# Kernel optimization log

Hardware: AMD Instinct MI355X
Metric: run time of the kernel (lower is better)

The kernel has to match this reference:

```python
import jax, jax.numpy as jnp
import numpy as np

B, C, H, W = 32, 512, 32, 32


def setup_inputs() -> dict:
    key = jax.random.key(0)
    ks = jax.random.split(key, 7)
    c2 = C // 2
    s_in = (1.0 / C) ** 0.5   # torch Conv2d default init scale (kernel 1x1)
    s_c2 = (1.0 / c2) ** 0.5
    return {
        "x": jax.random.normal(ks[0], (B, C, H, W), jnp.float32),
        "Wk": jax.random.normal(ks[1], (c2, C), jnp.float32) * s_in,
        "bk": jax.random.normal(ks[2], (c2,), jnp.float32) * s_in,
        "Wv": jax.random.normal(ks[3], (c2, C), jnp.float32) * s_in,
        "bv": jax.random.normal(ks[4], (c2,), jnp.float32) * s_in,
        "Wo": jax.random.normal(ks[5], (C, c2), jnp.float32) * s_c2,
        "bo": jax.random.normal(ks[6], (C,), jnp.float32) * s_c2,
    }


def reference(x, Wk, bk, Wv, bv, Wo, bo):
    Bn, Cn, Hn, Wn = x.shape
    c2 = Cn // 2
    M = Hn * Wn
    # 1x1 convs as channel contractions
    k = jnp.einsum('oc,bchw->bohw', Wk, x) + bk[None, :, None, None]   # [B,c2,H,W]
    v = jnp.einsum('oc,bchw->bohw', Wv, x) + bv[None, :, None, None]   # [B,c2,H,W]
    # torch .reshape(B, M, c2) reinterprets memory (NOT a transpose) -> same in jnp
    v = v.reshape(Bn, M, c2)                                           # [B,M,c2]
    kf = k.reshape(Bn, c2, M)                                          # [B,c2,M]
    # cov_feature: k^T I_hat k with I_hat = (1/M)I - (1/M^2)11^T
    #            = (1/M) k^T k - (1/M^2) s s^T,  s = sum over channels
    gram = jnp.einsum('bcm,bcn->bmn', kf, kf) / M                      # [B,M,M]
    s = kf.sum(axis=1)                                                 # [B,M]
    cov = gram - (s[:, :, None] * s[:, None, :]) / (M * M)
    attn = jax.nn.softmax(cov * (c2 ** -0.5), axis=-1)                 # [B,M,M]
    out = jnp.einsum('bmn,bnc->bmc', attn, v)                          # [B,M,c2]
    # torch .view(B, c2, H, W) is also a raw memory reinterpretation
    out = out.reshape(Bn, c2, Hn, Wn)
    out = jnp.einsum('oc,bchw->bohw', Wo, out) + bo[None, :, None, None]
    return out + x
```

## Files before the change

### kernel.cpp

```cpp
#include <hip/hip_runtime.h>


typedef short bf8 __attribute__((ext_vector_type(8)));
typedef float f32x4 __attribute__((ext_vector_type(4)));

#define MFMA16(a, b, c) __builtin_amdgcn_mfma_f32_16x16x32_bf16((a), (b), (c), 0, 0, 0)

__device__ __forceinline__ short f2bf(float x) {
  unsigned u = __float_as_uint(x);
  u += 0x7fffu + ((u >> 16) & 1u);
  return (short)(u >> 16);
}

__device__ __forceinline__ void gll16(const short* g, void* l) {
  __builtin_amdgcn_global_load_lds(
      (const __attribute__((address_space(1))) unsigned int*)g,
      (__attribute__((address_space(3))) unsigned int*)l, 16, 0, 0);
}

__device__ __forceinline__ void gemm_core(const short* __restrict__ A,
                                          const short* __restrict__ B,
                                          int ldA, int ldB, int ksteps,
                                          char* smem, f32x4 acc[4][4]) {
  const int tid = threadIdx.x;
  const int w = tid >> 6, l = tid & 63;
  const int q = l >> 4, i = l & 15;
  const int wm = w & 1, wn = w >> 1;
  const int srow = l >> 3;
  const int gcol = ((l & 7) ^ srow) * 8;
  f32x4 zz = {0.f, 0.f, 0.f, 0.f};
  #pragma unroll
  for (int mt = 0; mt < 4; ++mt)
    #pragma unroll
    for (int nt = 0; nt < 4; ++nt) acc[mt][nt] = zz;

  for (int ks = 0; ks < ksteps; ++ks) {
    __syncthreads();
    const short* Ak = A + ks * 64 + gcol;
    const short* Bk = B + ks * 64 + gcol;
    #pragma unroll
    for (int j = 0; j < 4; ++j) {
      int s = w * 4 + j;
      size_t row = (size_t)(s * 8 + srow);
      gll16(Ak + row * ldA, smem + s * 1024);
      gll16(Bk + row * ldB, smem + 16384 + s * 1024);
    }
    __syncthreads();
    #pragma unroll
    for (int kq = 0; kq < 2; ++kq) {
      int sw = ((kq * 4 + q) ^ (i & 7)) * 16;
      bf8 af[4], bq[4];
      #pragma unroll
      for (int mt = 0; mt < 4; ++mt)
        af[mt] = *(const bf8*)(smem + (wm * 64 + mt * 16 + i) * 128 + sw);
      #pragma unroll
      for (int nt = 0; nt < 4; ++nt)
        bq[nt] = *(const bf8*)(smem + 16384 + (wn * 64 + nt * 16 + i) * 128 + sw);
      #pragma unroll
      for (int mt = 0; mt < 4; ++mt)
        #pragma unroll
        for (int nt = 0; nt < 4; ++nt)
          acc[mt][nt] = MFMA16(af[mt], bq[nt], acc[mt][nt]);
    }
  }
}

__global__ __launch_bounds__(256) void p0_xpose(const float* __restrict__ x,
                                                short* __restrict__ xT) {
  __shared__ float lds[64][65];
  int cb = blockIdx.x, sb = blockIdx.y, b = blockIdx.z;
  int t = threadIdx.x;
  int c0 = cb * 64, sp0 = sb * 64;
  const float4* x4 = reinterpret_cast<const float4*>(x);
  #pragma unroll
  for (int j = 0; j < 4; ++j) {
    int lin = t + 256 * j;
    int cl = lin >> 4, s4 = lin & 15;
    float4 v = x4[(((size_t)b * 512 + c0 + cl) * 1024 + sp0 + s4 * 4) >> 2];
    lds[cl][s4 * 4 + 0] = v.x; lds[cl][s4 * 4 + 1] = v.y;
    lds[cl][s4 * 4 + 2] = v.z; lds[cl][s4 * 4 + 3] = v.w;
  }
  __syncthreads();
  int spl = t >> 2, cs = (t & 3) * 16;
  bf8 o0, o1;
  #pragma unroll
  for (int j = 0; j < 8; ++j) o0[j] = f2bf(lds[cs + j][spl]);
  #pragma unroll
  for (int j = 0; j < 8; ++j) o1[j] = f2bf(lds[cs + 8 + j][spl]);
  size_t base = ((size_t)b * 1024 + sp0 + spl) * 512 + c0 + cs;
  *reinterpret_cast<bf8*>(xT + base) = o0;
  *reinterpret_cast<bf8*>(xT + base + 8) = o1;
}

__global__ __launch_bounds__(256) void w0_weights(const float* __restrict__ Wk,
                                                  const float* __restrict__ Wv,
                                                  const float* __restrict__ Wo,
                                                  short* __restrict__ Wkv_bf,
                                                  short* __restrict__ Wo_bf) {
  int g = blockIdx.x * 256 + threadIdx.x;
  if (g < 262144) {
    int o = g >> 9, c = g & 511;
    float v = (o < 256) ? Wk[o * 512 + c] : Wv[(o - 256) * 512 + c];
    Wkv_bf[g] = f2bf(v);
  } else {
    int i2 = g - 262144;
    Wo_bf[i2] = f2bf(Wo[i2]);
  }
}

__global__ __launch_bounds__(256, 2) void k1_kv(const short* __restrict__ xT,
                                                const short* __restrict__ Wkv,
                                                const float* __restrict__ bk,
                                                const float* __restrict__ bv,
                                                short* __restrict__ kT,
                                                short* __restrict__ vT,
                                                float* __restrict__ s_part) {
  __shared__ __attribute__((aligned(16))) char smem[32768];
  f32x4 acc[4][4];
  int bm = blockIdx.x, bn = blockIdx.y;
  gemm_core(xT + (size_t)bm * 128 * 512, Wkv + (size_t)bn * 128 * 512,
            512, 512, 8, smem, acc);
  int tid = threadIdx.x;
  int w = tid >> 6, l = tid & 63, q = l >> 4, i = l & 15;
  int wm = w & 1, wn = w >> 1;
  int mbase = bm * 128 + wm * 64;
  int nbase = bn * 128 + wn * 64;
  if (bn < 2) {
    float rp[4][4];
    #pragma unroll
    for (int mt = 0; mt < 4; ++mt)
      #pragma unroll
      for (int r = 0; r < 4; ++r) rp[mt][r] = 0.f;
    #pragma unroll
    for (int mt = 0; mt < 4; ++mt)
      #pragma unroll
      for (int nt = 0; nt < 4; ++nt) {
        float bias = bk[nbase + nt * 16 + i];
        #pragma unroll
        for (int r = 0; r < 4; ++r) {
          float val = acc[mt][nt][r] + bias;
          int mg = mbase + mt * 16 + q * 4 + r;
          kT[(size_t)mg * 256 + nbase + nt * 16 + i] = f2bf(val);
          rp[mt][r] += val;
        }
      }
    #pragma unroll
    for (int mask = 1; mask <= 8; mask <<= 1)
      #pragma unroll
      for (int mt = 0; mt < 4; ++mt)
        #pragma unroll
        for (int r = 0; r < 4; ++r) rp[mt][r] += __shfl_xor(rp[mt][r], mask, 64);
    if (i == 0) {
      int pg = bn * 2 + wn;
      #pragma unroll
      for (int mt = 0; mt < 4; ++mt)
        #pragma unroll
        for (int r = 0; r < 4; ++r)
          s_part[pg * 32768 + mbase + mt * 16 + q * 4 + r] = rp[mt][r];
    }
  } else {
    #pragma unroll
    for (int mt = 0; mt < 4; ++mt)
      #pragma unroll
      for (int nt = 0; nt < 4; ++nt) {
        int o2 = nbase + nt * 16 + i - 256;
        float bias = bv[o2];
        #pragma unroll
        for (int r = 0; r < 4; ++r) {
          float val = acc[mt][nt][r] + bias;
          int mg = mbase + mt * 16 + q * 4 + r;
          int b = mg >> 10, sp = mg & 1023;
          vT[((size_t)b * 256 + (sp & 255)) * 1024 + 4 * o2 + (sp >> 8)] = f2bf(val);
        }
      }
  }
}

__global__ __launch_bounds__(256) void k1b_sum(const float* __restrict__ s_part,
                                               float* __restrict__ s_buf) {
  int t = blockIdx.x * 256 + threadIdx.x;
  s_buf[t] = s_part[t] + s_part[32768 + t] + s_part[65536 + t] + s_part[98304 + t];
}

__global__ __launch_bounds__(256, 2) void k2a_gram(const short* __restrict__ kT,
                                                   const float* __restrict__ s_buf,
                                                   short* __restrict__ P,
                                                   float* __restrict__ rsum_part) {
  __shared__ __attribute__((aligned(16))) char smem[36864];
  f32x4 acc[4][4];
  int bm = blockIdx.x, bn = blockIdx.y, b = blockIdx.z;
  const short* kb = kT + (size_t)b * 1024 * 256;
  gemm_core(kb + (size_t)bm * 128 * 256, kb + (size_t)bn * 128 * 256,
            256, 256, 4, smem, acc);
  int tid = threadIdx.x;
  int w = tid >> 6, l = tid & 63, q = l >> 4, i = l & 15;
  int wm = w & 1, wn = w >> 1;
  int mloc = bm * 128 + wm * 64, nloc = bn * 128 + wn * 64;
  const float sc1 = 1.0f / 16384.0f;
  const float sc2 = 1.0f / 16777216.0f;
  const float* sB = s_buf + b * 1024;
  float sm[4][4], sn[4];
  #pragma unroll
  for (int mt = 0; mt < 4; ++mt)
    #pragma unroll
    for (int r = 0; r < 4; ++r) sm[mt][r] = sB[mloc + mt * 16 + q * 4 + r];
  #pragma unroll
  for (int nt = 0; nt < 4; ++nt) sn[nt] = sB[nloc + nt * 16 + i];

  __syncthreads();
  short* pb = (short*)(smem + w * 9216);
  float rp[4][4];
  #pragma unroll
  for (int mt = 0; mt < 4; ++mt)
    #pragma unroll
    for (int r = 0; r < 4; ++r) rp[mt][r] = 0.f;
  #pragma unroll
  for (int mt = 0; mt < 4; ++mt)
    #pragma unroll
    for (int nt = 0; nt < 4; ++nt)
      #pragma unroll
      for (int r = 0; r < 4; ++r) {
        float p = __expf(acc[mt][nt][r] * sc1 - sm[mt][r] * sn[nt] * sc2);
        rp[mt][r] += p;
        pb[(mt * 16 + q * 4 + r) * 72 + nt * 16 + i] = f2bf(p);
      }
  #pragma unroll
  for (int mask = 1; mask <= 8; mask <<= 1)
    #pragma unroll
    for (int mt = 0; mt < 4; ++mt)
      #pragma unroll
      for (int r = 0; r < 4; ++r) rp[mt][r] += __shfl_xor(rp[mt][r], mask, 64);
  if (i == 0) {
    int pg = bn * 2 + wn;
    float* rpp = rsum_part + pg * 32768 + b * 1024;
    #pragma unroll
    for (int mt = 0; mt < 4; ++mt)
      #pragma unroll
      for (int r = 0; r < 4; ++r)
        rpp[mloc + mt * 16 + q * 4 + r] = rp[mt][r];
  }
  short* Pb = P + ((size_t)b * 1024 + mloc) * 1024 + nloc;
  #pragma unroll
  for (int j = 0; j < 8; ++j) {
    int row = j * 8 + (l >> 3), c = l & 7;
    bf8 vv = *(const bf8*)(pb + row * 72 + c * 8);
    *(bf8*)(Pb + (size_t)row * 1024 + c * 8) = vv;
  }
}

__global__ __launch_bounds__(256) void k2c_rinv(const float* __restrict__ rsum_part,
                                                float* __restrict__ rinv) {
  int t = blockIdx.x * 256 + threadIdx.x;
  float s = 0.f;
  #pragma unroll
  for (int pg = 0; pg < 16; ++pg) s += rsum_part[pg * 32768 + t];
  rinv[t] = 1.0f / s;
}

__global__ __launch_bounds__(256, 2) void k2b_pv(const short* __restrict__ P,
                                                 const short* __restrict__ vT,
                                                 const float* __restrict__ rinv,
                                                 short* __restrict__ OB) {
  __shared__ __attribute__((aligned(16))) char smem[32768];
  f32x4 acc[4][4];
  int bm = blockIdx.x, bn = blockIdx.y, b = blockIdx.z;
  gemm_core(P + ((size_t)b * 1024 + bm * 128) * 1024,
            vT + ((size_t)b * 256 + bn * 128) * 1024, 1024, 1024, 16, smem, acc);
  int tid = threadIdx.x;
  int w = tid >> 6, l = tid & 63, q = l >> 4, i = l & 15;
  int wm = w & 1, wn = w >> 1;
  int mloc = bm * 128 + wm * 64, cloc = bn * 128 + wn * 64;
  float ri[4][4];
  #pragma unroll
  for (int mt = 0; mt < 4; ++mt)
    #pragma unroll
    for (int r = 0; r < 4; ++r)
      ri[mt][r] = rinv[b * 1024 + mloc + mt * 16 + q * 4 + r];
  __syncthreads();
  short* ob = (short*)(smem + w * 8192);
  #pragma unroll
  for (int mt = 0; mt < 4; ++mt)
    #pragma unroll
    for (int nt = 0; nt < 4; ++nt)
      #pragma unroll
      for (int r = 0; r < 4; ++r) {
        int lr = r * 64 + nt * 16 + i;
        ob[lr * 16 + mt * 4 + q] = f2bf(acc[mt][nt][r] * ri[mt][r]);
      }
  short* obg = OB + (size_t)b * 1024 * 256;
  int colbase = mloc >> 2;
  #pragma unroll
  for (int j = 0; j < 8; ++j) {
    int lr = j * 32 + (l >> 1), ch = l & 1;
    bf8 vv = *(const bf8*)(ob + lr * 16 + ch * 8);
    int rr = lr >> 6, cc = lr & 63;
    *(bf8*)(obg + ((size_t)rr * 256 + cloc + cc) * 256 + colbase + ch * 8) = vv;
  }
}

__global__ __launch_bounds__(256, 2) void k3_out(const short* __restrict__ Wo_bf,
                                                 const short* __restrict__ OB,
                                                 const float* __restrict__ bo,
                                                 const float* __restrict__ x,
                                                 float* __restrict__ out) {
  __shared__ __attribute__((aligned(16))) char smem[32768];
  f32x4 acc[4][4];
  int bm = blockIdx.x, bn = blockIdx.y, b = blockIdx.z;
  gemm_core(Wo_bf + (size_t)bm * 128 * 256,
            OB + ((size_t)b * 1024 + bn * 128) * 256, 256, 256, 4, smem, acc);
  int tid = threadIdx.x;
  int w = tid >> 6, l = tid & 63, q = l >> 4, i = l & 15;
  int wm = w & 1, wn = w >> 1;
  int oloc = bm * 128 + wm * 64, sploc = bn * 128 + wn * 64;
  #pragma unroll
  for (int mt = 0; mt < 4; ++mt)
    #pragma unroll
    for (int r = 0; r < 4; ++r) {
      int o = oloc + mt * 16 + q * 4 + r;
      float bias = bo[o];
      #pragma unroll
      for (int nt = 0; nt < 4; ++nt) {
        int sp = sploc + nt * 16 + i;
        size_t idx = ((size_t)b * 512 + o) * 1024 + sp;
        out[idx] = acc[mt][nt][r] + bias + x[idx];
      }
    }
}

extern "C" void kernel_launch(void* const* d_in, const int* in_sizes, int n_in,
                              void* d_out, int out_size, void* d_ws, size_t ws_size,
                              hipStream_t stream) {
  (void)in_sizes; (void)n_in; (void)out_size; (void)ws_size;
  const float* x  = (const float*)d_in[0];
  const float* Wk = (const float*)d_in[1];
  const float* bk = (const float*)d_in[2];
  const float* Wv = (const float*)d_in[3];
  const float* bv = (const float*)d_in[4];
  const float* Wo = (const float*)d_in[5];
  const float* bo = (const float*)d_in[6];
  float* out = (float*)d_out;
  char* ws = (char*)d_ws;

  short* xT     = (short*)(ws);
  short* Pbuf   = (short*)(ws);
  short* kTb    = (short*)(ws + 67108864);
  short* OB     = (short*)(ws + 67108864);
  short* vTb    = (short*)(ws + 83886080);
  short* Wkv_bf = (short*)(ws + 100663296);
  short* Wo_bf  = (short*)(ws + 101187584);
  float* s_part = (float*)(ws + 101449728);
  float* s_buf  = (float*)(ws + 101974016);
  float* rsum_p = (float*)(ws + 102105088);
  float* rinv   = (float*)(ws + 104202240);

  p0_xpose<<<dim3(8, 16, 32), 256, 0, stream>>>(x, xT);
  w0_weights<<<1536, 256, 0, stream>>>(Wk, Wv, Wo, Wkv_bf, Wo_bf);
  k1_kv<<<dim3(256, 4), 256, 0, stream>>>(xT, Wkv_bf, bk, bv, kTb, vTb, s_part);
  k1b_sum<<<128, 256, 0, stream>>>(s_part, s_buf);
  k2a_gram<<<dim3(8, 8, 32), 256, 0, stream>>>(kTb, s_buf, Pbuf, rsum_p);
  k2c_rinv<<<128, 256, 0, stream>>>(rsum_p, rinv);
  k2b_pv<<<dim3(8, 2, 32), 256, 0, stream>>>(Pbuf, vTb, rinv, OB);
  k3_out<<<dim3(4, 8, 32), 256, 0, stream>>>(Wo_bf, OB, bo, x, out);
}
```

Before: 262.8 us.

## Fuse gram, softmax and PV into a flash-style kernel without materializing P

Replaces the gram/exp kernel, the row-sum reduction kernel and the PV GEMM with one kernel per (64-row tile, batch). It streams 128-column key tiles, computes exp scores into an LDS panel and accumulates P·V in registers, then normalises by row sums reduced in LDS. This removes the 64 MB bf16 P round trip through global memory and two kernel launches. In exchange the grid is only 512 blocks with 80 KB LDS each, the K tile is re-read per block, and there is no max-subtraction (same as before).

```diff
diff --git a/kernel.cpp b/kernel.cpp
--- a/kernel.cpp
+++ b/kernel.cpp
@@ -182,119 +182,176 @@
   s_buf[t] = s_part[t] + s_part[32768 + t] + s_part[65536 + t] + s_part[98304 + t];
 }
 
-__global__ __launch_bounds__(256, 2) void k2a_gram(const short* __restrict__ kT,
+__global__ __launch_bounds__(256, 2) void k2_fused(const short* __restrict__ kT,
+                                                   const short* __restrict__ vT,
                                                    const float* __restrict__ s_buf,
-                                                   short* __restrict__ P,
-                                                   float* __restrict__ rsum_part) {
-  __shared__ __attribute__((aligned(16))) char smem[36864];
-  f32x4 acc[4][4];
-  int bm = blockIdx.x, bn = blockIdx.y, b = blockIdx.z;
-  const short* kb = kT + (size_t)b * 1024 * 256;
-  gemm_core(kb + (size_t)bm * 128 * 256, kb + (size_t)bn * 128 * 256,
-            256, 256, 4, smem, acc);
-  int tid = threadIdx.x;
-  int w = tid >> 6, l = tid & 63, q = l >> 4, i = l & 15;
-  int wm = w & 1, wn = w >> 1;
-  int mloc = bm * 128 + wm * 64, nloc = bn * 128 + wn * 64;
+                                                   short* __restrict__ OB) {
+  __shared__ __attribute__((aligned(16))) char smem[81920];
+  char* Apan = smem;
+  char* Ppan = smem + 32768;
+  char* Bst  = smem + 49152;
+
+  const int bm = blockIdx.x, b = blockIdx.y;
+  const int tid = threadIdx.x;
+  const int w = tid >> 6, l = tid & 63;
+  const int q = l >> 4, i = l & 15;
+  const int srow = l >> 3;
+  const int gcol = ((l & 7) ^ srow) * 8;
+
+  const short* kTb = kT + (size_t)b * 1024 * 256;
+  const short* vTb = vT + (size_t)b * 256 * 1024;
+  const float* sB = s_buf + b * 1024;
+
+  {
+    const short* Am = kTb + (size_t)bm * 64 * 256;
+    #pragma unroll
+    for (int ks = 0; ks < 4; ++ks)
+      #pragma unroll
+      for (int j2 = 0; j2 < 2; ++j2) {
+        int s2 = w * 2 + j2;
+        gll16(Am + (size_t)(s2 * 8 + srow) * 256 + ks * 64 + gcol,
+              Apan + ks * 8192 + s2 * 1024);
+      }
+  }
+
+  float sm[4][4];
+  #pragma unroll
+  for (int mt = 0; mt < 4; ++mt)
+    #pragma unroll
+    for (int r = 0; r < 4; ++r) sm[mt][r] = sB[bm * 64 + mt * 16 + q * 4 + r];
+
+  f32x4 zz = {0.f, 0.f, 0.f, 0.f};
+  f32x4 acc_o[4][4];
+  #pragma unroll
+  for (int mt = 0; mt < 4; ++mt)
+    #pragma unroll
+    for (int ct = 0; ct < 4; ++ct) acc_o[mt][ct] = zz;
+  float rowsum[4][4];
+  #pragma unroll
+  for (int mt = 0; mt < 4; ++mt)
+    #pragma unroll
+    for (int r = 0; r < 4; ++r) rowsum[mt][r] = 0.f;
+
   const float sc1 = 1.0f / 16384.0f;
   const float sc2 = 1.0f / 16777216.0f;
-  const float* sB = s_buf + b * 1024;
-  float sm[4][4], sn[4];
-  #pragma unroll
-  for (int mt = 0; mt < 4; ++mt)
-    #pragma unroll
-    for (int r = 0; r < 4; ++r) sm[mt][r] = sB[mloc + mt * 16 + q * 4 + r];
-  #pragma unroll
-  for (int nt = 0; nt < 4; ++nt) sn[nt] = sB[nloc + nt * 16 + i];
-
+
+  for (int n0 = 0; n0 < 1024; n0 += 128) {
+    f32x4 acc_s[4][2];
+    #pragma unroll
+    for (int mt = 0; mt < 4; ++mt)
+      #pragma unroll
+      for (int nt = 0; nt < 2; ++nt) acc_s[mt][nt] = zz;
+    const short* Bn = kTb + (size_t)n0 * 256;
+    for (int ks = 0; ks < 4; ++ks) {
+      __syncthreads();
+      #pragma unroll
+      for (int j = 0; j < 4; ++j) {
+        int s = w * 4 + j;
+        gll16(Bn + (size_t)(s * 8 + srow) * 256 + ks * 64 + gcol, Bst + s * 1024);
+      }
+      __syncthreads();
+      #pragma unroll
+      for (int kq = 0; kq < 2; ++kq) {
+        int sw = ((kq * 4 + q) ^ (i & 7)) * 16;
+        bf8 af[4], bq2[2];
+        #pragma unroll
+        for (int mt = 0; mt < 4; ++mt)
+          af[mt] = *(const bf8*)(Apan + ks * 8192 + (mt * 16 + i) * 128 + sw);
+        #pragma unroll
+        for (int nt = 0; nt < 2; ++nt)
+          bq2[nt] = *(const bf8*)(Bst + (w * 32 + nt * 16 + i) * 128 + sw);
+        #pragma unroll
+        for (int mt = 0; mt < 4; ++mt)
+          #pragma unroll
+          for (int nt = 0; nt < 2; ++nt)
+            acc_s[mt][nt] = MFMA16(af[mt], bq2[nt], acc_s[mt][nt]);
+      }
+    }
+    float sn0 = sB[n0 + w * 32 + i];
+    float sn1 = sB[n0 + w * 32 + 16 + i];
+    #pragma unroll
+    for (int nt = 0; nt < 2; ++nt) {
+      float sn = nt ? sn1 : sn0;
+      int nl = w * 32 + nt * 16 + i;
+      char* pbase = Ppan + (nl >> 6) * 8192 + (nl & 7) * 2;
+      int gchunk = (nl >> 3) & 7;
+      #pragma unroll
+      for (int mt = 0; mt < 4; ++mt)
+        #pragma unroll
+        for (int r = 0; r < 4; ++r) {
+          int ml = mt * 16 + q * 4 + r;
+          float p = __expf(acc_s[mt][nt][r] * sc1 - sm[mt][r] * sn * sc2);
+          rowsum[mt][r] += p;
+          *(short*)(pbase + ml * 128 + ((gchunk ^ (ml & 7)) * 16)) = f2bf(p);
+        }
+    }
+    for (int ks2 = 0; ks2 < 2; ++ks2) {
+      __syncthreads();
+      #pragma unroll
+      for (int j = 0; j < 8; ++j) {
+        int s = w * 8 + j;
+        gll16(vTb + (size_t)(s * 8 + srow) * 1024 + n0 + ks2 * 64 + gcol,
+              Bst + s * 1024);
+      }
+      __syncthreads();
+      #pragma unroll
+      for (int kq = 0; kq < 2; ++kq) {
+        int sw = ((kq * 4 + q) ^ (i & 7)) * 16;
+        bf8 ap[4], bv4[4];
+        #pragma unroll
+        for (int mt = 0; mt < 4; ++mt)
+          ap[mt] = *(const bf8*)(Ppan + ks2 * 8192 + (mt * 16 + i) * 128 + sw);
+        #pragma unroll
+        for (int ct = 0; ct < 4; ++ct)
+          bv4[ct] = *(const bf8*)(Bst + (w * 64 + ct * 16 + i) * 128 + sw);
+        #pragma unroll
+        for (int mt = 0; mt < 4; ++mt)
+          #pragma unroll
+          for (int ct = 0; ct < 4; ++ct)
+            acc_o[mt][ct] = MFMA16(ap[mt], bv4[ct], acc_o[mt][ct]);
+      }
+    }
+  }
+  #pragma unroll
+  for (int mask = 1; mask <= 8; mask <<= 1)
+    #pragma unroll
+    for (int mt = 0; mt < 4; ++mt)
+      #pragma unroll
+      for (int r = 0; r < 4; ++r) rowsum[mt][r] += __shfl_xor(rowsum[mt][r], mask, 64);
   __syncthreads();
-  short* pb = (short*)(smem + w * 9216);
-  float rp[4][4];
-  #pragma unroll
-  for (int mt = 0; mt < 4; ++mt)
-    #pragma unroll
-    for (int r = 0; r < 4; ++r) rp[mt][r] = 0.f;
-  #pragma unroll
-  for (int mt = 0; mt < 4; ++mt)
-    #pragma unroll
-    for (int nt = 0; nt < 4; ++nt)
-      #pragma unroll
-      for (int r = 0; r < 4; ++r) {
-        float p = __expf(acc[mt][nt][r] * sc1 - sm[mt][r] * sn[nt] * sc2);
-        rp[mt][r] += p;
-        pb[(mt * 16 + q * 4 + r) * 72 + nt * 16 + i] = f2bf(p);
-      }
-  #pragma unroll
-  for (int mask = 1; mask <= 8; mask <<= 1)
-    #pragma unroll
-    for (int mt = 0; mt < 4; ++mt)
-      #pragma unroll
-      for (int r = 0; r < 4; ++r) rp[mt][r] += __shfl_xor(rp[mt][r], mask, 64);
+  float* rs = (float*)Ppan;
   if (i == 0) {
-    int pg = bn * 2 + wn;
-    float* rpp = rsum_part + pg * 32768 + b * 1024;
     #pragma unroll
     for (int mt = 0; mt < 4; ++mt)
       #pragma unroll
       for (int r = 0; r < 4; ++r)
-        rpp[mloc + mt * 16 + q * 4 + r] = rp[mt][r];
-  }
-  short* Pb = P + ((size_t)b * 1024 + mloc) * 1024 + nloc;
-  #pragma unroll
-  for (int j = 0; j < 8; ++j) {
-    int row = j * 8 + (l >> 3), c = l & 7;
-    bf8 vv = *(const bf8*)(pb + row * 72 + c * 8);
-    *(bf8*)(Pb + (size_t)row * 1024 + c * 8) = vv;
-  }
-}
-
-__global__ __launch_bounds__(256) void k2c_rinv(const float* __restrict__ rsum_part,
-                                                float* __restrict__ rinv) {
-  int t = blockIdx.x * 256 + threadIdx.x;
-  float s = 0.f;
-  #pragma unroll
-  for (int pg = 0; pg < 16; ++pg) s += rsum_part[pg * 32768 + t];
-  rinv[t] = 1.0f / s;
-}
-
-__global__ __launch_bounds__(256, 2) void k2b_pv(const short* __restrict__ P,
-                                                 const short* __restrict__ vT,
-                                                 const float* __restrict__ rinv,
-                                                 short* __restrict__ OB) {
-  __shared__ __attribute__((aligned(16))) char smem[32768];
-  f32x4 acc[4][4];
-  int bm = blockIdx.x, bn = blockIdx.y, b = blockIdx.z;
-  gemm_core(P + ((size_t)b * 1024 + bm * 128) * 1024,
-            vT + ((size_t)b * 256 + bn * 128) * 1024, 1024, 1024, 16, smem, acc);
-  int tid = threadIdx.x;
-  int w = tid >> 6, l = tid & 63, q = l >> 4, i = l & 15;
-  int wm = w & 1, wn = w >> 1;
-  int mloc = bm * 128 + wm * 64, cloc = bn * 128 + wn * 64;
-  float ri[4][4];
-  #pragma unroll
-  for (int mt = 0; mt < 4; ++mt)
-    #pragma unroll
-    for (int r = 0; r < 4; ++r)
-      ri[mt][r] = rinv[b * 1024 + mloc + mt * 16 + q * 4 + r];
+        rs[w * 64 + mt * 16 + q * 4 + r] = rowsum[mt][r];
+  }
   __syncthreads();
-  short* ob = (short*)(smem + w * 8192);
-  #pragma unroll
-  for (int mt = 0; mt < 4; ++mt)
-    #pragma unroll
-    for (int nt = 0; nt < 4; ++nt)
-      #pragma unroll
-      for (int r = 0; r < 4; ++r) {
-        int lr = r * 64 + nt * 16 + i;
-        ob[lr * 16 + mt * 4 + q] = f2bf(acc[mt][nt][r] * ri[mt][r]);
-      }
+  float rinv[4][4];
+  #pragma unroll
+  for (int mt = 0; mt < 4; ++mt)
+    #pragma unroll
+    for (int r = 0; r < 4; ++r) {
+      int m = mt * 16 + q * 4 + r;
+      rinv[mt][r] = 1.0f / (rs[m] + rs[64 + m] + rs[128 + m] + rs[192 + m]);
+    }
+  short* ob = (short*)(Bst + w * 8192);
+  #pragma unroll
+  for (int mt = 0; mt < 4; ++mt)
+    #pragma unroll
+    for (int ct = 0; ct < 4; ++ct)
+      #pragma unroll
+      for (int r = 0; r < 4; ++r)
+        ob[(r * 64 + ct * 16 + i) * 16 + mt * 4 + q] =
+            f2bf(acc_o[mt][ct][r] * rinv[mt][r]);
   short* obg = OB + (size_t)b * 1024 * 256;
-  int colbase = mloc >> 2;
-  #pragma unroll
-  for (int j = 0; j < 8; ++j) {
-    int lr = j * 32 + (l >> 1), ch = l & 1;
+  #pragma unroll
+  for (int jj = 0; jj < 8; ++jj) {
+    int lr = jj * 32 + (l >> 1), ch = l & 1;
     bf8 vv = *(const bf8*)(ob + lr * 16 + ch * 8);
     int rr = lr >> 6, cc = lr & 63;
-    *(bf8*)(obg + ((size_t)rr * 256 + cloc + cc) * 256 + colbase + ch * 8) = vv;
+    *(bf8*)(obg + ((size_t)(rr * 256 + w * 64 + cc)) * 256 + bm * 16 + ch * 8) = vv;
   }
 }
 
@@ -342,23 +399,18 @@
   char* ws = (char*)d_ws;
 
   short* xT     = (short*)(ws);
-  short* Pbuf   = (short*)(ws);
-  short* kTb    = (short*)(ws + 67108864);
-  short* OB     = (short*)(ws + 67108864);
-  short* vTb    = (short*)(ws + 83886080);
-  short* Wkv_bf = (short*)(ws + 100663296);
-  short* Wo_bf  = (short*)(ws + 101187584);
-  float* s_part = (float*)(ws + 101449728);
-  float* s_buf  = (float*)(ws + 101974016);
-  float* rsum_p = (float*)(ws + 102105088);
-  float* rinv   = (float*)(ws + 104202240);
+  short* OB     = (short*)(ws);
+  short* kTb    = (short*)(ws + 33554432);
+  short* vTb    = (short*)(ws + 50331648);
+  short* Wkv_bf = (short*)(ws + 67108864);
+  short* Wo_bf  = (short*)(ws + 67633152);
+  float* s_part = (float*)(ws + 67895296);
+  float* s_buf  = (float*)(ws + 68419584);
 
   p0_xpose<<<dim3(8, 16, 32), 256, 0, stream>>>(x, xT);
   w0_weights<<<1536, 256, 0, stream>>>(Wk, Wv, Wo, Wkv_bf, Wo_bf);
   k1_kv<<<dim3(256, 4), 256, 0, stream>>>(xT, Wkv_bf, bk, bv, kTb, vTb, s_part);
   k1b_sum<<<128, 256, 0, stream>>>(s_part, s_buf);
-  k2a_gram<<<dim3(8, 8, 32), 256, 0, stream>>>(kTb, s_buf, Pbuf, rsum_p);
-  k2c_rinv<<<128, 256, 0, stream>>>(rsum_p, rinv);
-  k2b_pv<<<dim3(8, 2, 32), 256, 0, stream>>>(Pbuf, vTb, rinv, OB);
+  k2_fused<<<dim3(16, 32), 256, 0, stream>>>(kTb, vTb, s_buf, OB);
   k3_out<<<dim3(4, 8, 32), 256, 0, stream>>>(Wo_bf, OB, bo, x, out);
 }
```

Result: faster. 252.2 us (-4.0%).
